# Optimization experiments

Hardware: AMD Instinct MI355X
Metric: run time of the kernel (lower is better)

The kernel has to match this reference:

```python
import jax, jax.numpy as jnp
import numpy as np

B = 2_000_000

def setup_inputs() -> dict:
    key = jax.random.key(0)
    k1, k2 = jax.random.split(key)
    output = jax.random.uniform(k1, (B, 25), dtype=jnp.float32)
    label_mask = jax.random.uniform(k2, (B, 25), dtype=jnp.float32)
    return {"output": output, "label_mask": label_mask}

def returning_rate(output, label_mask):
    # pred/mask: [B, 5, 5] -- 5-tier x 5-slot probability grid per sample
    pred = output.reshape(-1, 5, 5)
    mask = label_mask.reshape(-1, 5, 5)
    p = lambda i, j: pred[:, i, j]
    m = lambda i, j: mask[:, i, j]
    zeros = jnp.zeros_like(p(0, 0))

    # p1: chained retrieval-rehandle probabilities (mask multiplies only the
    # last product term, exactly matching the original operator precedence)
    p1_1 = p(4, 0) * p(4, 1) * m(3, 1)
    p1_2 = p(4, 0) * p(4, 2) + p(3, 1) * p(3, 2) * m(2, 2)
    p1_3 = p(4, 0) * p(4, 3) + p(3, 1) * p(3, 3) + p(2, 2) * p(2, 3) * m(1, 3)
    p1_4 = (p(4, 0) * p(4, 4) + p(3, 1) * p(3, 4) + p(2, 2) * p(2, 4)
            + p(1, 3) * p(1, 4) * m(0, 4))
    p_1 = jnp.stack([zeros, p1_1, p1_2, p1_3, p1_4], axis=1)  # [B, 5]

    # p2: complement-chain probabilities
    q40 = 1.0 - p(4, 0)
    q31 = 1.0 - p(3, 1)
    q22 = 1.0 - p(2, 2)
    q13 = 1.0 - p(1, 3)
    p2_1 = q31 * (1.0 - q40) * m(3, 1)
    p2_2 = q22 * (1.0 - q40 * q31) * m(2, 2)
    p2_3 = q13 * (1.0 - q40 * q31 * q22) * m(1, 3)
    p2_4 = (1.0 - p(0, 4)) * (1.0 - q40 * q31 * q22 * q13) * m(0, 4)
    p_2 = jnp.stack([zeros, p2_1, p2_2, p2_3, p2_4], axis=1)  # [B, 5]
    return p_1, p_2

def reference(output, label_mask):
    return returning_rate(output, label_mask)
```

## Files before the change

### kernel.cpp

```cpp
#include <hip/hip_runtime.h>

__global__ void returning_rate_kernel(const float* __restrict__ pred,
                                      const float* __restrict__ mask,
                                      float* __restrict__ out, int B) {
    int idx = blockIdx.x * blockDim.x + threadIdx.x;
    int stride = gridDim.x * blockDim.x;
    for (int s = idx; s < B; s += stride) {
        const float* pr = pred + (size_t)s * 25;
        const float* mk = mask + (size_t)s * 25;

        float p40 = pr[20], p41 = pr[21], p42 = pr[22], p43 = pr[23], p44 = pr[24];
        float p31 = pr[16], p32 = pr[17], p33 = pr[18], p34 = pr[19];
        float p22 = pr[12], p23 = pr[13], p24 = pr[14];
        float p13 = pr[8],  p14 = pr[9];
        float p04 = pr[4];
        float m31 = mk[16], m22 = mk[12], m13 = mk[8], m04 = mk[4];

        float p1_1 = p40 * p41 * m31;
        float p1_2 = p40 * p42 + p31 * p32 * m22;
        float p1_3 = p40 * p43 + p31 * p33 + p22 * p23 * m13;
        float p1_4 = p40 * p44 + p31 * p34 + p22 * p24 + p13 * p14 * m04;

        float q40 = 1.f - p40, q31 = 1.f - p31, q22 = 1.f - p22, q13 = 1.f - p13;
        float p2_1 = q31 * (1.f - q40) * m31;
        float p2_2 = q22 * (1.f - q40 * q31) * m22;
        float p2_3 = q13 * (1.f - q40 * q31 * q22) * m13;
        float p2_4 = (1.f - p04) * (1.f - q40 * q31 * q22 * q13) * m04;

        float* o1 = out + (size_t)s * 5;
        o1[0] = 0.f; o1[1] = p1_1; o1[2] = p1_2; o1[3] = p1_3; o1[4] = p1_4;
        float* o2 = out + (size_t)B * 5 + (size_t)s * 5;
        o2[0] = 0.f; o2[1] = p2_1; o2[2] = p2_2; o2[3] = p2_3; o2[4] = p2_4;
    }
}

extern "C" void kernel_launch(void* const* d_in, const int* in_sizes, int n_in,
                              void* d_out, int out_size, void* d_ws, size_t ws_size,
                              hipStream_t stream) {
    const float* pred = (const float*)d_in[0];
    const float* mask = (const float*)d_in[1];
    float* out = (float*)d_out;
    int B = in_sizes[0] / 25;

    const int block = 256;
    int blocks = (B + block - 1) / block;
    if (blocks > 8192) blocks = 8192;
    returning_rate_kernel<<<blocks, block, 0, stream>>>(pred, mask, out, B);
}
```

Baseline: 92.55 us.

## Stage rows through shared memory for coalesced float4 loads and stores

Each block cooperatively loads a 256-row tile of pred and then mask into shared memory with float4 loads, extracts the needed fields per thread, computes results, and writes both outputs back through shared memory as coalesced float4 stores. It replaces strided per-thread global accesses with coalesced ones and drops the grid-stride loop for one block per tile. It adds several barriers, a large LDS footprint that may limit occupancy, and reads all 25 columns of both inputs.

```diff
diff --git a/kernel.cpp b/kernel.cpp
--- a/kernel.cpp
+++ b/kernel.cpp
@@ -1,49 +1,115 @@
 #include <hip/hip_runtime.h>
 
-__global__ void returning_rate_kernel(const float* __restrict__ pred,
-                                      const float* __restrict__ mask,
-                                      float* __restrict__ out, int B) {
-    int idx = blockIdx.x * blockDim.x + threadIdx.x;
-    int stride = gridDim.x * blockDim.x;
-    for (int s = idx; s < B; s += stride) {
-        const float* pr = pred + (size_t)s * 25;
-        const float* mk = mask + (size_t)s * 25;
+#define TILE 256
+#define TFLOATS (TILE * 25)
 
-        float p40 = pr[20], p41 = pr[21], p42 = pr[22], p43 = pr[23], p44 = pr[24];
-        float p31 = pr[16], p32 = pr[17], p33 = pr[18], p34 = pr[19];
-        float p22 = pr[12], p23 = pr[13], p24 = pr[14];
-        float p13 = pr[8],  p14 = pr[9];
-        float p04 = pr[4];
-        float m31 = mk[16], m22 = mk[12], m13 = mk[8], m04 = mk[4];
+__global__ __launch_bounds__(256) void returning_rate_kernel(
+    const float* __restrict__ pred, const float* __restrict__ mask,
+    float* __restrict__ out, int B) {
+  __shared__ float tile[TFLOATS];
+  const int t = threadIdx.x;
+  const long long blockRow = (long long)blockIdx.x * TILE;
+  const bool full = (blockRow + TILE <= (long long)B);
+  const bool active = (blockRow + t) < (long long)B;
 
-        float p1_1 = p40 * p41 * m31;
-        float p1_2 = p40 * p42 + p31 * p32 * m22;
-        float p1_3 = p40 * p43 + p31 * p33 + p22 * p23 * m13;
-        float p1_4 = p40 * p44 + p31 * p34 + p22 * p24 + p13 * p14 * m04;
+  if (full) {
+    const float4* src = (const float4*)(pred + blockRow * 25);
+    float4* dst = (float4*)tile;
+    #pragma unroll
+    for (int k = 0; k < 7; ++k) {
+      int i = k * 256 + t;
+      if (i < TFLOATS / 4) dst[i] = src[i];
+    }
+  } else {
+    const float* src = pred + blockRow * 25;
+    int n = (int)((long long)B - blockRow) * 25;
+    for (int i = t; i < n; i += 256) tile[i] = src[i];
+  }
+  __syncthreads();
 
-        float q40 = 1.f - p40, q31 = 1.f - p31, q22 = 1.f - p22, q13 = 1.f - p13;
-        float p2_1 = q31 * (1.f - q40) * m31;
-        float p2_2 = q22 * (1.f - q40 * q31) * m22;
-        float p2_3 = q13 * (1.f - q40 * q31 * q22) * m13;
-        float p2_4 = (1.f - p04) * (1.f - q40 * q31 * q22 * q13) * m04;
+  float p40=0,p41=0,p42=0,p43=0,p44=0,p31=0,p32=0,p33=0,p34=0;
+  float p22=0,p23=0,p24=0,p13=0,p14=0,p04=0;
+  if (active) {
+    const float* r = tile + t * 25;
+    p40=r[20]; p41=r[21]; p42=r[22]; p43=r[23]; p44=r[24];
+    p31=r[16]; p32=r[17]; p33=r[18]; p34=r[19];
+    p22=r[12]; p23=r[13]; p24=r[14];
+    p13=r[8];  p14=r[9];
+    p04=r[4];
+  }
+  __syncthreads();
 
-        float* o1 = out + (size_t)s * 5;
-        o1[0] = 0.f; o1[1] = p1_1; o1[2] = p1_2; o1[3] = p1_3; o1[4] = p1_4;
-        float* o2 = out + (size_t)B * 5 + (size_t)s * 5;
-        o2[0] = 0.f; o2[1] = p2_1; o2[2] = p2_2; o2[3] = p2_3; o2[4] = p2_4;
+  if (full) {
+    const float4* src = (const float4*)(mask + blockRow * 25);
+    float4* dst = (float4*)tile;
+    #pragma unroll
+    for (int k = 0; k < 7; ++k) {
+      int i = k * 256 + t;
+      if (i < TFLOATS / 4) dst[i] = src[i];
     }
+  } else {
+    const float* src = mask + blockRow * 25;
+    int n = (int)((long long)B - blockRow) * 25;
+    for (int i = t; i < n; i += 256) tile[i] = src[i];
+  }
+  __syncthreads();
+
+  float m31=0, m22=0, m13=0, m04=0;
+  if (active) {
+    const float* r = tile + t * 25;
+    m31=r[16]; m22=r[12]; m13=r[8]; m04=r[4];
+  }
+  __syncthreads();
+
+  float p1_1 = p40 * p41 * m31;
+  float p1_2 = p40 * p42 + p31 * p32 * m22;
+  float p1_3 = p40 * p43 + p31 * p33 + p22 * p23 * m13;
+  float p1_4 = p40 * p44 + p31 * p34 + p22 * p24 + p13 * p14 * m04;
+
+  float q40 = 1.f - p40, q31 = 1.f - p31, q22 = 1.f - p22, q13 = 1.f - p13;
+  float p2_1 = q31 * (1.f - q40) * m31;
+  float p2_2 = q22 * (1.f - q40 * q31) * m22;
+  float p2_3 = q13 * (1.f - q40 * q31 * q22) * m13;
+  float p2_4 = (1.f - p04) * (1.f - q40 * q31 * q22 * q13) * m04;
+
+  if (active) {
+    float* o1 = tile + t * 5;
+    o1[0]=0.f; o1[1]=p1_1; o1[2]=p1_2; o1[3]=p1_3; o1[4]=p1_4;
+    float* o2 = tile + TILE * 5 + t * 5;
+    o2[0]=0.f; o2[1]=p2_1; o2[2]=p2_2; o2[3]=p2_3; o2[4]=p2_4;
+  }
+  __syncthreads();
+
+  long long base1 = blockRow * 5;
+  long long base2 = (long long)B * 5 + blockRow * 5;
+  bool aligned = (((size_t)out | (size_t)(base2 * 4)) & 15) == 0;
+  if (full && aligned) {
+    float4* o1 = (float4*)(out + base1);
+    float4* o2 = (float4*)(out + base2);
+    const float4* s1 = (const float4*)tile;
+    const float4* s2 = (const float4*)(tile + TILE * 5);
+    #pragma unroll
+    for (int k = 0; k < 2; ++k) {
+      int i = k * 256 + t;
+      if (i < TILE * 5 / 4) { o1[i] = s1[i]; o2[i] = s2[i]; }
+    }
+  } else {
+    int n = full ? TILE * 5 : (int)((long long)B - blockRow) * 5;
+    for (int i = t; i < n; i += 256) {
+      out[base1 + i] = tile[i];
+      out[base2 + i] = tile[TILE * 5 + i];
+    }
+  }
 }
 
 extern "C" void kernel_launch(void* const* d_in, const int* in_sizes, int n_in,
                               void* d_out, int out_size, void* d_ws, size_t ws_size,
                               hipStream_t stream) {
-    const float* pred = (const float*)d_in[0];
-    const float* mask = (const float*)d_in[1];
-    float* out = (float*)d_out;
-    int B = in_sizes[0] / 25;
+  const float* pred = (const float*)d_in[0];
+  const float* mask = (const float*)d_in[1];
+  float* out = (float*)d_out;
+  int B = in_sizes[0] / 25;
 
-    const int block = 256;
-    int blocks = (B + block - 1) / block;
-    if (blocks > 8192) blocks = 8192;
-    returning_rate_kernel<<<blocks, block, 0, stream>>>(pred, mask, out, B);
+  int blocks = (B + TILE - 1) / TILE;
+  returning_rate_kernel<<<blocks, 256, 0, stream>>>(pred, mask, out, B);
 }
```

After: 99.28 us. 1.07x slower.

## Process four rows per thread with aligned float4 loads and stores

Applied to the files above, without the earlier changes.

Each thread now handles four consecutive samples, whose combined 100-float block is 16-byte aligned. This lets the prediction rows be read with float4 loads and the outputs written with float4 stores. The intent is to cut memory instruction count and improve coalescing on this bandwidth-bound kernel. It also replaces the grid-stride loop with a full grid and adds a scalar tail path, at the cost of extra register use and some over-fetch of unused columns.

```diff
diff --git a/kernel.cpp b/kernel.cpp
--- a/kernel.cpp
+++ b/kernel.cpp
@@ -1,49 +1,92 @@
 #include <hip/hip_runtime.h>
 
-__global__ void returning_rate_kernel(const float* __restrict__ pred,
-                                      const float* __restrict__ mask,
-                                      float* __restrict__ out, int B) {
-    int idx = blockIdx.x * blockDim.x + threadIdx.x;
-    int stride = gridDim.x * blockDim.x;
-    for (int s = idx; s < B; s += stride) {
-        const float* pr = pred + (size_t)s * 25;
-        const float* mk = mask + (size_t)s * 25;
+__device__ __forceinline__ void row_math(
+    float p04, float p13, float p14, float p22, float p23, float p24,
+    float p31, float p32, float p33, float p34,
+    float p40, float p41, float p42, float p43, float p44,
+    float m31, float m22, float m13, float m04,
+    float* r1, float* r2) {
+  r1[0] = 0.f;
+  r1[1] = p40 * p41 * m31;
+  r1[2] = p40 * p42 + p31 * p32 * m22;
+  r1[3] = p40 * p43 + p31 * p33 + p22 * p23 * m13;
+  r1[4] = p40 * p44 + p31 * p34 + p22 * p24 + p13 * p14 * m04;
+  float q40 = 1.f - p40, q31 = 1.f - p31, q22 = 1.f - p22, q13 = 1.f - p13;
+  r2[0] = 0.f;
+  r2[1] = q31 * (1.f - q40) * m31;
+  r2[2] = q22 * (1.f - q40 * q31) * m22;
+  r2[3] = q13 * (1.f - q40 * q31 * q22) * m13;
+  r2[4] = (1.f - p04) * (1.f - q40 * q31 * q22 * q13) * m04;
+}
 
-        float p40 = pr[20], p41 = pr[21], p42 = pr[22], p43 = pr[23], p44 = pr[24];
-        float p31 = pr[16], p32 = pr[17], p33 = pr[18], p34 = pr[19];
-        float p22 = pr[12], p23 = pr[13], p24 = pr[14];
-        float p13 = pr[8],  p14 = pr[9];
-        float p04 = pr[4];
-        float m31 = mk[16], m22 = mk[12], m13 = mk[8], m04 = mk[4];
+__global__ __launch_bounds__(256) void returning_rate_kernel(
+    const float* __restrict__ pred, const float* __restrict__ mask,
+    float* __restrict__ out, int B) {
+  long long u = (long long)blockIdx.x * blockDim.x + threadIdx.x;
+  long long row0 = u * 4;
+  if (row0 >= B) return;
 
-        float p1_1 = p40 * p41 * m31;
-        float p1_2 = p40 * p42 + p31 * p32 * m22;
-        float p1_3 = p40 * p43 + p31 * p33 + p22 * p23 * m13;
-        float p1_4 = p40 * p44 + p31 * p34 + p22 * p24 + p13 * p14 * m04;
+  if (row0 + 4 <= B) {
+    const float* prBase = pred + row0 * 25;
+    const float* mkBase = mask + row0 * 25;
+    float o1v[20], o2v[20];
 
-        float q40 = 1.f - p40, q31 = 1.f - p31, q22 = 1.f - p22, q13 = 1.f - p13;
-        float p2_1 = q31 * (1.f - q40) * m31;
-        float p2_2 = q22 * (1.f - q40 * q31) * m22;
-        float p2_3 = q13 * (1.f - q40 * q31 * q22) * m13;
-        float p2_4 = (1.f - p04) * (1.f - q40 * q31 * q22 * q13) * m04;
+    #pragma unroll
+    for (int r = 0; r < 4; ++r) {
+      float a[24];
+      #pragma unroll
+      for (int c = 0; c < 6; ++c) {
+        float4 v;
+        __builtin_memcpy(&v, prBase + (6 * r + 1 + c) * 4, 16);
+        a[c * 4 + 0] = v.x; a[c * 4 + 1] = v.y;
+        a[c * 4 + 2] = v.z; a[c * 4 + 3] = v.w;
+      }
+      float m04 = mkBase[25 * r + 4];
+      float m13 = mkBase[25 * r + 8];
+      float m22 = mkBase[25 * r + 12];
+      float m31 = mkBase[25 * r + 16];
 
-        float* o1 = out + (size_t)s * 5;
-        o1[0] = 0.f; o1[1] = p1_1; o1[2] = p1_2; o1[3] = p1_3; o1[4] = p1_4;
-        float* o2 = out + (size_t)B * 5 + (size_t)s * 5;
-        o2[0] = 0.f; o2[1] = p2_1; o2[2] = p2_2; o2[3] = p2_3; o2[4] = p2_4;
+      row_math(a[r + 0],
+               a[r + 4],  a[r + 5],
+               a[r + 8],  a[r + 9],  a[r + 10],
+               a[r + 12], a[r + 13], a[r + 14], a[r + 15],
+               a[r + 16], a[r + 17], a[r + 18], a[r + 19], a[r + 20],
+               m31, m22, m13, m04,
+               &o1v[5 * r], &o2v[5 * r]);
     }
+
+    float* o1 = out + row0 * 5;
+    float* o2 = out + (size_t)B * 5 + row0 * 5;
+    #pragma unroll
+    for (int k = 0; k < 5; ++k) {
+      __builtin_memcpy(o1 + 4 * k, &o1v[4 * k], 16);
+      __builtin_memcpy(o2 + 4 * k, &o2v[4 * k], 16);
+    }
+  } else {
+    for (long long s = row0; s < B; ++s) {
+      const float* pr = pred + s * 25;
+      const float* mk = mask + s * 25;
+      float r1[5], r2[5];
+      row_math(pr[4], pr[8], pr[9], pr[12], pr[13], pr[14],
+               pr[16], pr[17], pr[18], pr[19],
+               pr[20], pr[21], pr[22], pr[23], pr[24],
+               mk[16], mk[12], mk[8], mk[4], r1, r2);
+      float* o1 = out + s * 5;
+      float* o2 = out + (size_t)B * 5 + s * 5;
+      for (int k = 0; k < 5; ++k) { o1[k] = r1[k]; o2[k] = r2[k]; }
+    }
+  }
 }
 
 extern "C" void kernel_launch(void* const* d_in, const int* in_sizes, int n_in,
                               void* d_out, int out_size, void* d_ws, size_t ws_size,
                               hipStream_t stream) {
-    const float* pred = (const float*)d_in[0];
-    const float* mask = (const float*)d_in[1];
-    float* out = (float*)d_out;
-    int B = in_sizes[0] / 25;
+  const float* pred = (const float*)d_in[0];
+  const float* mask = (const float*)d_in[1];
+  float* out = (float*)d_out;
+  int B = in_sizes[0] / 25;
 
-    const int block = 256;
-    int blocks = (B + block - 1) / block;
-    if (blocks > 8192) blocks = 8192;
-    returning_rate_kernel<<<blocks, block, 0, stream>>>(pred, mask, out, B);
+  long long threads = ((long long)B + 3) / 4;
+  int blocks = (int)((threads + 255) / 256);
+  returning_rate_kernel<<<blocks, 256, 0, stream>>>(pred, mask, out, B);
 }
```

New measurement: 177.8 us. 1.92x slower.

## Stage outputs in shared memory and write coalesced nontemporal float4 stores

Applied to the files above, without the earlier changes.

Each thread writes its two 5-float output rows into shared memory, and after a barrier the block writes them to global memory as contiguous float4 nontemporal stores. This replaces the strided scalar stores, which have a 20-byte stride per thread. The launch also drops the grid-stride loop and uses one block per 256-row tile. Input loads stay strided and uncoalesced, and the block now pays an extra shared-memory round trip and a barrier.

```diff
diff --git a/kernel.cpp b/kernel.cpp
--- a/kernel.cpp
+++ b/kernel.cpp
@@ -1,49 +1,75 @@
 #include <hip/hip_runtime.h>
 
-__global__ void returning_rate_kernel(const float* __restrict__ pred,
-                                      const float* __restrict__ mask,
-                                      float* __restrict__ out, int B) {
-    int idx = blockIdx.x * blockDim.x + threadIdx.x;
-    int stride = gridDim.x * blockDim.x;
-    for (int s = idx; s < B; s += stride) {
-        const float* pr = pred + (size_t)s * 25;
-        const float* mk = mask + (size_t)s * 25;
+#define TILE 256
 
-        float p40 = pr[20], p41 = pr[21], p42 = pr[22], p43 = pr[23], p44 = pr[24];
-        float p31 = pr[16], p32 = pr[17], p33 = pr[18], p34 = pr[19];
-        float p22 = pr[12], p23 = pr[13], p24 = pr[14];
-        float p13 = pr[8],  p14 = pr[9];
-        float p04 = pr[4];
-        float m31 = mk[16], m22 = mk[12], m13 = mk[8], m04 = mk[4];
+typedef float f32x4 __attribute__((ext_vector_type(4)));
 
-        float p1_1 = p40 * p41 * m31;
-        float p1_2 = p40 * p42 + p31 * p32 * m22;
-        float p1_3 = p40 * p43 + p31 * p33 + p22 * p23 * m13;
-        float p1_4 = p40 * p44 + p31 * p34 + p22 * p24 + p13 * p14 * m04;
+__global__ __launch_bounds__(256) void returning_rate_kernel(
+    const float* __restrict__ pred, const float* __restrict__ mask,
+    float* __restrict__ out, int B) {
+  __shared__ float o1s[TILE * 5];
+  __shared__ float o2s[TILE * 5];
 
-        float q40 = 1.f - p40, q31 = 1.f - p31, q22 = 1.f - p22, q13 = 1.f - p13;
-        float p2_1 = q31 * (1.f - q40) * m31;
-        float p2_2 = q22 * (1.f - q40 * q31) * m22;
-        float p2_3 = q13 * (1.f - q40 * q31 * q22) * m13;
-        float p2_4 = (1.f - p04) * (1.f - q40 * q31 * q22 * q13) * m04;
+  const int t = threadIdx.x;
+  const long long blockRow = (long long)blockIdx.x * TILE;
+  const long long s = blockRow + t;
+  const int nrows = (int)((blockRow + TILE <= (long long)B) ? TILE : ((long long)B - blockRow));
 
-        float* o1 = out + (size_t)s * 5;
-        o1[0] = 0.f; o1[1] = p1_1; o1[2] = p1_2; o1[3] = p1_3; o1[4] = p1_4;
-        float* o2 = out + (size_t)B * 5 + (size_t)s * 5;
-        o2[0] = 0.f; o2[1] = p2_1; o2[2] = p2_2; o2[3] = p2_3; o2[4] = p2_4;
-    }
+  if (t < nrows) {
+    const float* pr = pred + s * 25;
+    const float* mk = mask + s * 25;
+
+    float p40 = pr[20], p41 = pr[21], p42 = pr[22], p43 = pr[23], p44 = pr[24];
+    float p31 = pr[16], p32 = pr[17], p33 = pr[18], p34 = pr[19];
+    float p22 = pr[12], p23 = pr[13], p24 = pr[14];
+    float p13 = pr[8],  p14 = pr[9];
+    float p04 = pr[4];
+    float m31 = mk[16], m22 = mk[12], m13 = mk[8], m04 = mk[4];
+
+    float p1_1 = p40 * p41 * m31;
+    float p1_2 = p40 * p42 + p31 * p32 * m22;
+    float p1_3 = p40 * p43 + p31 * p33 + p22 * p23 * m13;
+    float p1_4 = p40 * p44 + p31 * p34 + p22 * p24 + p13 * p14 * m04;
+
+    float q40 = 1.f - p40, q31 = 1.f - p31, q22 = 1.f - p22, q13 = 1.f - p13;
+    float p2_1 = q31 * (1.f - q40) * m31;
+    float p2_2 = q22 * (1.f - q40 * q31) * m22;
+    float p2_3 = q13 * (1.f - q40 * q31 * q22) * m13;
+    float p2_4 = (1.f - p04) * (1.f - q40 * q31 * q22 * q13) * m04;
+
+    float* a = o1s + t * 5;
+    a[0] = 0.f; a[1] = p1_1; a[2] = p1_2; a[3] = p1_3; a[4] = p1_4;
+    float* b = o2s + t * 5;
+    b[0] = 0.f; b[1] = p2_1; b[2] = p2_2; b[3] = p2_3; b[4] = p2_4;
+  }
+  __syncthreads();
+
+  const int nfloats = nrows * 5;
+  const int nv4 = nfloats / 4;
+  float* g1 = out + blockRow * 5;
+  float* g2 = out + (long long)B * 5 + blockRow * 5;
+
+  for (int i = t; i < nv4; i += 256) {
+    f32x4 v1, v2;
+    __builtin_memcpy(&v1, &o1s[i * 4], 16);
+    __builtin_memcpy(&v2, &o2s[i * 4], 16);
+    __builtin_nontemporal_store(v1, (f32x4*)g1 + i);
+    __builtin_nontemporal_store(v2, (f32x4*)g2 + i);
+  }
+  for (int i = nv4 * 4 + t; i < nfloats; i += 256) {
+    g1[i] = o1s[i];
+    g2[i] = o2s[i];
+  }
 }
 
 extern "C" void kernel_launch(void* const* d_in, const int* in_sizes, int n_in,
                               void* d_out, int out_size, void* d_ws, size_t ws_size,
                               hipStream_t stream) {
-    const float* pred = (const float*)d_in[0];
-    const float* mask = (const float*)d_in[1];
-    float* out = (float*)d_out;
-    int B = in_sizes[0] / 25;
+  const float* pred = (const float*)d_in[0];
+  const float* mask = (const float*)d_in[1];
+  float* out = (float*)d_out;
+  int B = in_sizes[0] / 25;
 
-    const int block = 256;
-    int blocks = (B + block - 1) / block;
-    if (blocks > 8192) blocks = 8192;
-    returning_rate_kernel<<<blocks, block, 0, stream>>>(pred, mask, out, B);
+  int blocks = (int)(((long long)B + TILE - 1) / TILE);
+  returning_rate_kernel<<<blocks, 256, 0, stream>>>(pred, mask, out, B);
 }
```

After: 88.41 us, median of 2. 1.05x faster.
